# Kernel optimization log

Measured on AMD Instinct MI355X. Metric: run time of the kernel, lower is better.

The kernel has to match this reference:

```python
import jax, jax.numpy as jnp
import numpy as np

HEADS = 4
GROUPS = 32
EPS = 1e-5


def setup_inputs() -> dict:
    key = jax.random.key(0)
    ks = jax.random.split(key, 3)
    B, C, H, W = 8, 256, 32, 32
    x = jax.random.normal(ks[0], (B, C, H, W), dtype=jnp.float32)
    gamma = jnp.ones((C,), jnp.float32)
    beta = jnp.zeros((C,), jnp.float32)
    w_qkv = jax.random.normal(ks[1], (3 * C, C), jnp.float32) * (1.0 / np.sqrt(C))
    b_qkv = jnp.zeros((3 * C,), jnp.float32)
    w_proj = jax.random.normal(ks[2], (C, C), jnp.float32) * (1.0 / np.sqrt(C))
    b_proj = jnp.zeros((C,), jnp.float32)
    return {"x": x, "gamma": gamma, "beta": beta, "w_qkv": w_qkv,
            "b_qkv": b_qkv, "w_proj": w_proj, "b_proj": b_proj}


def group_norm(x, gamma, beta):
    B, C, H, W = x.shape
    xg = x.reshape(B, GROUPS, C // GROUPS, H, W)
    mean = xg.mean(axis=(2, 3, 4), keepdims=True)
    var = xg.var(axis=(2, 3, 4), keepdims=True)
    xg = (xg - mean) * jax.lax.rsqrt(var + EPS)
    xn = xg.reshape(B, C, H, W)
    return xn * gamma[None, :, None, None] + beta[None, :, None, None]


def reference(x, gamma, beta, w_qkv, b_qkv, w_proj, b_proj):
    B, C, H, W = x.shape
    hd = C // HEADS  # head dim
    h = group_norm(x, gamma, beta)
    # 1x1 conv == channel matmul: [B,3C,H,W]
    qkv = jnp.einsum('oc,bchw->bohw', w_qkv, h) + b_qkv[None, :, None, None]
    qkv = qkv.reshape(B, 3, HEADS, hd, H * W)
    q, k, v = qkv[:, 0], qkv[:, 1], qkv[:, 2]  # each [B, heads, hd, HW]
    attn = jnp.einsum('bhci,bhcj->bhij', q, k) * (hd ** -0.5)
    attn = jax.nn.softmax(attn, axis=-1)
    out = jnp.einsum('bhij,bhcj->bhci', attn, v).reshape(B, C, H, W)
    proj = jnp.einsum('oc,bchw->bohw', w_proj, out) + b_proj[None, :, None, None]
    return x + proj
```

## Files before the change

kernel.cpp:

```cpp
#include <hip/hip_runtime.h>
#include <hip/hip_bf16.h>

static constexpr int kC = 256;
static constexpr int kN = 1024;

using s16x8 = __attribute__((ext_vector_type(8))) short;
using f32x4 = __attribute__((ext_vector_type(4))) float;

__device__ inline f32x4 mfma16(s16x8 a, s16x8 b, f32x4 c) {
  return __builtin_amdgcn_mfma_f32_16x16x32_bf16(a, b, c, 0, 0, 0);
}

__device__ inline unsigned short f2bf(float f) {
  unsigned u = __builtin_bit_cast(unsigned, f);
  u = (u + 0x7fffu + ((u >> 16) & 1u)) >> 16;
  return (unsigned short)u;
}

__device__ inline float exp2_fast(float x) {
  float r;
  asm("v_exp_f32 %0, %1" : "=v"(r) : "v"(x));
  return r;
}

__device__ inline unsigned cvt_pk_bf16(float lo, float hi) {
  unsigned r;
  asm("v_cvt_pk_bf16_f32 %0, %1, %2" : "=v"(r) : "v"(lo), "v"(hi));
  return r;
}

static constexpr float kQScale = 0.18033688011112042f;

__global__ __launch_bounds__(256) void prep_kernel(
    const float* __restrict__ x, const float* __restrict__ gamma,
    const float* __restrict__ beta, unsigned short* __restrict__ hTp,
    const float* __restrict__ wq, const float* __restrict__ wp,
    unsigned short* __restrict__ Wqp, unsigned short* __restrict__ Wpp) {
  if (blockIdx.x < 128) {
    const int tid = blockIdx.x * 256 + threadIdx.x;
    const float* src;
    unsigned short* dst;
    if (tid < 24576) {
      const int fragid = tid >> 6, lane = tid & 63;
      const int Mt = fragid >> 3, kt = fragid & 7;
      src = wq + (size_t)(Mt * 16 + (lane & 15)) * 256 + kt * 32 + (lane >> 4) * 8;
      dst = Wqp + (size_t)tid * 8;
    } else {
      const int id = tid - 24576;
      const int fragid = id >> 6, lane = id & 63;
      const int Mt = fragid >> 3, kt = fragid & 7;
      src = wp + (size_t)(Mt * 16 + (lane & 15)) * 256 + kt * 32 + (lane >> 4) * 8;
      dst = Wpp + (size_t)id * 8;
    }
    const float4 f0 = *(const float4*)src;
    const float4 f1 = *(const float4*)(src + 4);
    ushort4 o0, o1;
    o0.x = f2bf(f0.x); o0.y = f2bf(f0.y); o0.z = f2bf(f0.z); o0.w = f2bf(f0.w);
    o1.x = f2bf(f1.x); o1.y = f2bf(f1.y); o1.z = f2bf(f1.z); o1.w = f2bf(f1.w);
    *(ushort4*)dst = o0;
    *(ushort4*)(dst + 4) = o1;
    return;
  }

  const int bg = blockIdx.x - 128;
  const int b = bg >> 5, g = bg & 31;
  const size_t base = ((size_t)b * kC + (size_t)g * 8) * kN;
  const float4* __restrict__ x4 = (const float4*)(x + base);
  const int t = threadIdx.x;

  float vv[8][4];
  float s = 0.f, ss = 0.f;
#pragma unroll
  for (int i = 0; i < 8; ++i) {
    const float4 v = x4[t + 256 * i];
    vv[i][0] = v.x; vv[i][1] = v.y; vv[i][2] = v.z; vv[i][3] = v.w;
    s += v.x + v.y + v.z + v.w;
    ss += v.x * v.x + v.y * v.y + v.z * v.z + v.w * v.w;
  }
#pragma unroll
  for (int off = 32; off > 0; off >>= 1) {
    s += __shfl_xor(s, off);
    ss += __shfl_xor(ss, off);
  }
  __shared__ float rs[4], rss[4];
  const int wave = t >> 6, lane = t & 63;
  if (lane == 0) { rs[wave] = s; rss[wave] = ss; }
  __syncthreads();
  s = rs[0] + rs[1] + rs[2] + rs[3];
  ss = rss[0] + rss[1] + rss[2] + rss[3];
  const float mean = s * (1.f / 8192.f);
  const float var = ss * (1.f / 8192.f) - mean * mean;
  const float rinv = rsqrtf(var + 1e-5f);
  float ga[8], be[8];
#pragma unroll
  for (int i = 0; i < 8; ++i) {
    ga[i] = gamma[g * 8 + i] * rinv;
    be[i] = beta[g * 8 + i] - mean * ga[i];
  }
  const int kt = g >> 2, gq = g & 3;
#pragma unroll
  for (int r = 0; r < 4; ++r) {
    const int pos = 4 * t + r;
    const int nt = pos >> 4, lp = pos & 15;
    unsigned short* dst =
        hTp + ((size_t)((b * 64 + nt) * 8 + kt) * 64 + (gq * 16 + lp)) * 8;
    ushort4 o0, o1;
    o0.x = f2bf(vv[0][r] * ga[0] + be[0]);
    o0.y = f2bf(vv[1][r] * ga[1] + be[1]);
    o0.z = f2bf(vv[2][r] * ga[2] + be[2]);
    o0.w = f2bf(vv[3][r] * ga[3] + be[3]);
    o1.x = f2bf(vv[4][r] * ga[4] + be[4]);
    o1.y = f2bf(vv[5][r] * ga[5] + be[5]);
    o1.z = f2bf(vv[6][r] * ga[6] + be[6]);
    o1.w = f2bf(vv[7][r] * ga[7] + be[7]);
    *(ushort4*)dst = o0;
    *(ushort4*)(dst + 4) = o1;
  }
}

__device__ inline void gload(const s16x8* __restrict__ Af,
                             const s16x8* __restrict__ Bf,
                             int Mt0, int Nt0, int kt, int lane,
                             s16x8 (&a)[4], s16x8 (&bb)[2]) {
#pragma unroll
  for (int mt = 0; mt < 4; ++mt)
    a[mt] = Af[((size_t)(Mt0 + mt) * 8 + kt) * 64 + lane];
#pragma unroll
  for (int nt = 0; nt < 2; ++nt)
    bb[nt] = Bf[((size_t)(Nt0 + nt) * 8 + kt) * 64 + lane];
}

__device__ inline void gmfma(const s16x8 (&a)[4], const s16x8 (&bb)[2],
                             f32x4 (&acc)[4][2], bool swap) {
  if (swap) {
#pragma unroll
    for (int mt = 0; mt < 4; ++mt)
#pragma unroll
      for (int nt = 0; nt < 2; ++nt)
        acc[mt][nt] = mfma16(bb[nt], a[mt], acc[mt][nt]);
  } else {
#pragma unroll
    for (int mt = 0; mt < 4; ++mt)
#pragma unroll
      for (int nt = 0; nt < 2; ++nt)
        acc[mt][nt] = mfma16(a[mt], bb[nt], acc[mt][nt]);
  }
}

template <int MT128, bool PROJ>
__global__ __launch_bounds__(256) void gemm_pk_kernel(
    const unsigned short* __restrict__ Wp, const float* __restrict__ bias,
    const unsigned short* __restrict__ Bp,
    unsigned short* __restrict__ Qp, unsigned short* __restrict__ Kp,
    unsigned short* __restrict__ Vp,
    const float* __restrict__ res, float* __restrict__ outp) {
  constexpr int CPX = MT128 * 16;
  const int bid = blockIdx.x;
  const int swz = (bid & 7) * CPX + (bid >> 3);
  const int b = swz / CPX, rr = swz % CPX;
  const int mb = rr >> 4, nb = rr & 15;
  const int t = threadIdx.x;
  const int wave = t >> 6, lane = t & 63;
  const int li = lane & 15, grp = lane >> 4;
  const int m0 = mb * 128 + (wave >> 1) * 64;
  const int n0 = nb * 64 + (wave & 1) * 32;
  const bool swap = (!PROJ) && (mb >= 4);
  const int Mt0 = m0 >> 4;
  const int Nt0 = b * 64 + (n0 >> 4);
  const s16x8* __restrict__ Af = (const s16x8*)Wp;
  const s16x8* __restrict__ Bf = (const s16x8*)Bp;

  f32x4 acc[4][2];
#pragma unroll
  for (int mt = 0; mt < 4; ++mt)
#pragma unroll
    for (int nt = 0; nt < 2; ++nt) acc[mt][nt] = f32x4{0.f, 0.f, 0.f, 0.f};

  s16x8 sa[3][4], sb[3][2];
  gload(Af, Bf, Mt0, Nt0, 0, lane, sa[0], sb[0]);
  gload(Af, Bf, Mt0, Nt0, 1, lane, sa[1], sb[1]);
#pragma unroll
  for (int kt = 0; kt < 8; ++kt) {
    if (kt + 2 < 8)
      gload(Af, Bf, Mt0, Nt0, kt + 2, lane, sa[(kt + 2) % 3], sb[(kt + 2) % 3]);
    gmfma(sa[kt % 3], sb[kt % 3], acc, swap);
  }

  if (PROJ) {
#pragma unroll
    for (int mt = 0; mt < 4; ++mt) {
      const int mbase = m0 + mt * 16 + 4 * grp;
      const float4 bv = *(const float4*)(bias + mbase);
      const float bvr[4] = {bv.x, bv.y, bv.z, bv.w};
#pragma unroll
      for (int nt = 0; nt < 2; ++nt) {
        const int pos = n0 + nt * 16 + li;
#pragma unroll
        for (int r = 0; r < 4; ++r) {
          const size_t ob = ((size_t)(b * 256 + mbase + r)) * 1024 + pos;
          outp[ob] = acc[mt][nt][r] + bvr[r] + res[ob];
        }
      }
    }
  } else if (!swap) {
    unsigned short* __restrict__ Tp = (mb < 2) ? Qp : Kp;
    const float qs = (mb < 2) ? kQScale : 1.0f;
#pragma unroll
    for (int mt = 0; mt < 4; ++mt) {
      const int mbase = m0 + mt * 16;
      const int head = (mbase >> 6) & 3;
      const int bh = b * 4 + head;
      const int c16 = mbase & 63;
      const int ks = c16 >> 5;
      const int grpp = ((c16 >> 3) + (grp >> 1)) & 3;
      const float4 bv = *(const float4*)(bias + mbase + 4 * grp);
#pragma unroll
      for (int nt = 0; nt < 2; ++nt) {
        const int pt = (n0 >> 4) + nt;
        ushort4 o;
        o.x = f2bf((acc[mt][nt][0] + bv.x) * qs);
        o.y = f2bf((acc[mt][nt][1] + bv.y) * qs);
        o.z = f2bf((acc[mt][nt][2] + bv.z) * qs);
        o.w = f2bf((acc[mt][nt][3] + bv.w) * qs);
        *(ushort4*)(Tp + (size_t)bh * 65536 +
                    ((size_t)(pt * 2 + ks) * 64 + grpp * 16 + li) * 8 +
                    (grp & 1) * 4) = o;
      }
    }
  } else {
#pragma unroll
    for (int mt = 0; mt < 4; ++mt) {
      const int mbase = m0 + mt * 16;
      const int head = (mbase >> 6) & 3;
      const int bh = b * 4 + head;
      const int ct = (mbase & 63) >> 4;
      const float bvc = bias[mbase + li];
      const int kvt = n0 >> 5;
#pragma unroll
      for (int nt = 0; nt < 2; ++nt) {
        const int grpv = (nt * 2 + (grp >> 1)) & 3;
        ushort4 o;
        o.x = f2bf(acc[mt][nt][0] + bvc);
        o.y = f2bf(acc[mt][nt][1] + bvc);
        o.z = f2bf(acc[mt][nt][2] + bvc);
        o.w = f2bf(acc[mt][nt][3] + bvc);
        *(ushort4*)(Vp + (size_t)bh * 65536 +
                    ((size_t)(ct * 32 + kvt) * 64 + grpv * 16 + li) * 8 +
                    (grp & 1) * 4) = o;
      }
    }
  }
}

__global__ __launch_bounds__(256) void attn_mfma_kernel(
    const unsigned short* __restrict__ Qp, const unsigned short* __restrict__ Kp,
    const unsigned short* __restrict__ Vp, unsigned short* __restrict__ aoTp) {
  __shared__ unsigned short P_lds[4][16][56];
  const int bid = blockIdx.x;
  const int swz = (bid & 7) * 64 + (bid >> 3);
  const int bh = swz >> 4, qb = swz & 15;
  const int b = bh >> 2, head = bh & 3;
  const int t = threadIdx.x;
  const int wave = t >> 6, lane = t & 63;
  const int li = lane & 15, grp = lane >> 4;
  const int q0 = qb * 64 + wave * 16;
  const unsigned short* __restrict__ Qb = Qp + (size_t)bh * 65536;
  const unsigned short* __restrict__ Kb = Kp + (size_t)bh * 65536;
  const unsigned short* __restrict__ Vb = Vp + (size_t)bh * 65536;

  s16x8 qf[2];
#pragma unroll
  for (int ks = 0; ks < 2; ++ks)
    qf[ks] = *(const s16x8*)(Qb + (((q0 >> 4) * 2 + ks) * 64 + lane) * 8);

  f32x4 O[4];
#pragma unroll
  for (int ct = 0; ct < 4; ++ct) O[ct] = f32x4{0.f, 0.f, 0.f, 0.f};
  f32x4 lvec = f32x4{0.f, 0.f, 0.f, 0.f};
  float m_run = -1.0e30f;

  auto loadK = [&](int it, s16x8 (&kk)[2][2]) {
#pragma unroll
    for (int mt = 0; mt < 2; ++mt)
#pragma unroll
      for (int ks = 0; ks < 2; ++ks)
        kk[mt][ks] = *(const s16x8*)(
            Kb + ((size_t)((it * 2 + mt) * 2 + ks) * 64 + lane) * 8);
  };
  auto loadV = [&](int it, s16x8 (&vv)[4]) {
#pragma unroll
    for (int ct = 0; ct < 4; ++ct)
      vv[ct] = *(const s16x8*)(Vb + ((size_t)(ct * 32 + it) * 64 + lane) * 8);
  };
  auto qkt = [&](const s16x8 (&kk)[2][2], f32x4 (&s)[2]) {
#pragma unroll
    for (int mt = 0; mt < 2; ++mt) {
      s[mt] = mfma16(kk[mt][0], qf[0], f32x4{0.f, 0.f, 0.f, 0.f});
      s[mt] = mfma16(kk[mt][1], qf[1], s[mt]);
    }
  };
  auto smaxpv = [&](f32x4 (&s)[2], const s16x8 (&vv)[4]) {
    const float A = fmaxf(fmaxf(s[0][0], s[0][1]), s[0][2]);
    const float B = fmaxf(fmaxf(s[0][3], s[1][0]), s[1][1]);
    const float C = fmaxf(fmaxf(s[1][2], s[1][3]), A);
    float pm = fmaxf(B, C);
    pm = fmaxf(pm, __shfl_xor(pm, 16));
    pm = fmaxf(pm, __shfl_xor(pm, 32));
    if (!__all(pm <= m_run + 8.0f)) {
      const float mnew = fmaxf(m_run, pm);
      const float f = exp2_fast(m_run - mnew);
      m_run = mnew;
      lvec *= f;
#pragma unroll
      for (int ct = 0; ct < 4; ++ct) O[ct] *= f;
    }
    f32x4 p[2];
#pragma unroll
    for (int mt = 0; mt < 2; ++mt) {
#pragma unroll
      for (int r = 0; r < 4; ++r) p[mt][r] = exp2_fast(s[mt][r] - m_run);
      lvec += p[mt];
    }
#pragma unroll
    for (int mt = 0; mt < 2; ++mt) {
      uint2 cc;
      cc.x = cvt_pk_bf16(p[mt][0], p[mt][1]);
      cc.y = cvt_pk_bf16(p[mt][2], p[mt][3]);
      *(uint2*)&P_lds[wave][li][16 * mt + 4 * grp] = cc;
    }
    const s16x8 pf = *(const s16x8*)&P_lds[wave][li][8 * grp];
#pragma unroll
    for (int ct = 0; ct < 4; ++ct) O[ct] = mfma16(vv[ct], pf, O[ct]);
  };

  s16x8 k0[2][2], k1[2][2], v0[4], v1[4];
  loadK(0, k0);
  loadV(0, v0);
  f32x4 sc[2];
  qkt(k0, sc);
  loadK(1, k1);

#pragma unroll 1
  for (int h2 = 0; h2 < 16; ++h2) {
    const int tt = 2 * h2;
    loadV(tt + 1, v1);
    f32x4 sn[2];
    qkt(k1, sn);
    loadK(tt + 2, k0);
    smaxpv(sc, v0);
    loadV(tt + 2, v0);
    f32x4 s2[2];
    qkt(k0, s2);
    loadK(tt + 3, k1);
    smaxpv(sn, v1);
    sc[0] = s2[0];
    sc[1] = s2[1];
  }

  float lt = lvec[0] + lvec[1] + lvec[2] + lvec[3];
  lt += __shfl_xor(lt, 16);
  lt += __shfl_xor(lt, 32);
  const float rinv = 1.f / lt;
#pragma unroll
  for (int ct = 0; ct < 4; ++ct) {
    const int ktp = head * 2 + (ct >> 1);
    const int grpp = ((ct & 1) * 2 + (grp >> 1)) & 3;
    ushort4 o;
    o.x = f2bf(O[ct][0] * rinv);
    o.y = f2bf(O[ct][1] * rinv);
    o.z = f2bf(O[ct][2] * rinv);
    o.w = f2bf(O[ct][3] * rinv);
    *(ushort4*)(aoTp +
                ((size_t)((b * 64 + (q0 >> 4)) * 8 + ktp) * 64 + grpp * 16 + li) * 8 +
                (grp & 1) * 4) = o;
  }
}

extern "C" void kernel_launch(void* const* d_in, const int* in_sizes, int n_in,
                              void* d_out, int out_size, void* d_ws, size_t ws_size,
                              hipStream_t stream) {
  const float* x      = (const float*)d_in[0];
  const float* gamma  = (const float*)d_in[1];
  const float* beta   = (const float*)d_in[2];
  const float* w_qkv  = (const float*)d_in[3];
  const float* b_qkv  = (const float*)d_in[4];
  const float* w_proj = (const float*)d_in[5];
  const float* b_proj = (const float*)d_in[6];
  float* out = (float*)d_out;

  unsigned short* ws = (unsigned short*)d_ws;
  unsigned short* Wqp  = ws;
  unsigned short* Wpp  = Wqp + 196608;
  unsigned short* hTp  = Wpp + 65536;
  unsigned short* Qp   = hTp + 2097152;
  unsigned short* Kp   = Qp + 2097152;
  unsigned short* Vp   = Kp + 2097152;
  unsigned short* aoTp = Vp + 2097152;

  hipLaunchKernelGGL(prep_kernel, dim3(384), dim3(256), 0, stream,
                     x, gamma, beta, hTp, w_qkv, w_proj, Wqp, Wpp);
  hipLaunchKernelGGL((gemm_pk_kernel<6, false>), dim3(768), dim3(256), 0, stream,
                     Wqp, b_qkv, hTp, Qp, Kp, Vp, nullptr, nullptr);
  hipLaunchKernelGGL(attn_mfma_kernel, dim3(512), dim3(256), 0, stream,
                     Qp, Kp, Vp, aoTp);
  hipLaunchKernelGGL((gemm_pk_kernel<2, true>), dim3(256), dim3(256), 0, stream,
                     Wpp, b_proj, aoTp, nullptr, nullptr, nullptr, x, out);
}
```

Measured before the change: 43.06 us.

## Fuse output projection into attention kernel via LDS-staged attention output

The attention kernel now uses 512-thread blocks that cover all four heads for 32 query positions. The normalized attention output is staged in shared memory and multiplied by the projection weights in the same kernel, with the bias and residual added there. This removes a kernel launch and the global write and read of the intermediate attention output. In exchange there are half as many blocks, larger blocks, a block-wide barrier, and more LDS per block, which may lower occupancy and parallelism in the attention phase.

```diff
diff --git a/kernel.cpp b/kernel.cpp
--- a/kernel.cpp
+++ b/kernel.cpp
@@ -147,24 +147,21 @@
   }
 }
 
-template <int MT128, bool PROJ>
-__global__ __launch_bounds__(256) void gemm_pk_kernel(
+__global__ __launch_bounds__(256) void gemm_qkv_kernel(
     const unsigned short* __restrict__ Wp, const float* __restrict__ bias,
     const unsigned short* __restrict__ Bp,
     unsigned short* __restrict__ Qp, unsigned short* __restrict__ Kp,
-    unsigned short* __restrict__ Vp,
-    const float* __restrict__ res, float* __restrict__ outp) {
-  constexpr int CPX = MT128 * 16;
+    unsigned short* __restrict__ Vp) {
   const int bid = blockIdx.x;
-  const int swz = (bid & 7) * CPX + (bid >> 3);
-  const int b = swz / CPX, rr = swz % CPX;
+  const int swz = (bid & 7) * 96 + (bid >> 3);
+  const int b = swz / 96, rr = swz % 96;
   const int mb = rr >> 4, nb = rr & 15;
   const int t = threadIdx.x;
   const int wave = t >> 6, lane = t & 63;
   const int li = lane & 15, grp = lane >> 4;
   const int m0 = mb * 128 + (wave >> 1) * 64;
   const int n0 = nb * 64 + (wave & 1) * 32;
-  const bool swap = (!PROJ) && (mb >= 4);
+  const bool swap = mb >= 4;
   const int Mt0 = m0 >> 4;
   const int Nt0 = b * 64 + (n0 >> 4);
   const s16x8* __restrict__ Af = (const s16x8*)Wp;
@@ -186,23 +183,7 @@
     gmfma(sa[kt % 3], sb[kt % 3], acc, swap);
   }
 
-  if (PROJ) {
-#pragma unroll
-    for (int mt = 0; mt < 4; ++mt) {
-      const int mbase = m0 + mt * 16 + 4 * grp;
-      const float4 bv = *(const float4*)(bias + mbase);
-      const float bvr[4] = {bv.x, bv.y, bv.z, bv.w};
-#pragma unroll
-      for (int nt = 0; nt < 2; ++nt) {
-        const int pos = n0 + nt * 16 + li;
-#pragma unroll
-        for (int r = 0; r < 4; ++r) {
-          const size_t ob = ((size_t)(b * 256 + mbase + r)) * 1024 + pos;
-          outp[ob] = acc[mt][nt][r] + bvr[r] + res[ob];
-        }
-      }
-    }
-  } else if (!swap) {
+  if (!swap) {
     unsigned short* __restrict__ Tp = (mb < 2) ? Qp : Kp;
     const float qs = (mb < 2) ? kQScale : 1.0f;
 #pragma unroll
@@ -252,18 +233,22 @@
   }
 }
 
-__global__ __launch_bounds__(256) void attn_mfma_kernel(
+__global__ __launch_bounds__(512) void attn_proj_kernel(
     const unsigned short* __restrict__ Qp, const unsigned short* __restrict__ Kp,
-    const unsigned short* __restrict__ Vp, unsigned short* __restrict__ aoTp) {
-  __shared__ unsigned short P_lds[4][16][56];
+    const unsigned short* __restrict__ Vp, const unsigned short* __restrict__ Wpp,
+    const float* __restrict__ bpj, const float* __restrict__ x,
+    float* __restrict__ out) {
+  __shared__ unsigned short P_lds[8][16][56];
+  __shared__ __align__(16) unsigned short Ex[2][8][64][8];
   const int bid = blockIdx.x;
-  const int swz = (bid & 7) * 64 + (bid >> 3);
-  const int bh = swz >> 4, qb = swz & 15;
-  const int b = bh >> 2, head = bh & 3;
+  const int swz = (bid & 7) * 32 + (bid >> 3);
+  const int b = swz >> 5, qb = swz & 31;
   const int t = threadIdx.x;
-  const int wave = t >> 6, lane = t & 63;
+  const int w8 = t >> 6, lane = t & 63;
+  const int head = w8 & 3, qh = w8 >> 2;
   const int li = lane & 15, grp = lane >> 4;
-  const int q0 = qb * 64 + wave * 16;
+  const int q0 = qb * 32 + qh * 16;
+  const int bh = b * 4 + head;
   const unsigned short* __restrict__ Qb = Qp + (size_t)bh * 65536;
   const unsigned short* __restrict__ Kb = Kp + (size_t)bh * 65536;
   const unsigned short* __restrict__ Vb = Vp + (size_t)bh * 65536;
@@ -326,9 +311,9 @@
       uint2 cc;
       cc.x = cvt_pk_bf16(p[mt][0], p[mt][1]);
       cc.y = cvt_pk_bf16(p[mt][2], p[mt][3]);
-      *(uint2*)&P_lds[wave][li][16 * mt + 4 * grp] = cc;
-    }
-    const s16x8 pf = *(const s16x8*)&P_lds[wave][li][8 * grp];
+      *(uint2*)&P_lds[w8][li][16 * mt + 4 * grp] = cc;
+    }
+    const s16x8 pf = *(const s16x8*)&P_lds[w8][li][8 * grp];
 #pragma unroll
     for (int ct = 0; ct < 4; ++ct) O[ct] = mfma16(vv[ct], pf, O[ct]);
   };
@@ -370,9 +355,56 @@
     o.y = f2bf(O[ct][1] * rinv);
     o.z = f2bf(O[ct][2] * rinv);
     o.w = f2bf(O[ct][3] * rinv);
-    *(ushort4*)(aoTp +
-                ((size_t)((b * 64 + (q0 >> 4)) * 8 + ktp) * 64 + grpp * 16 + li) * 8 +
-                (grp & 1) * 4) = o;
+    *(ushort4*)&Ex[qh][ktp][grpp * 16 + li][(grp & 1) * 4] = o;
+  }
+  __syncthreads();
+
+  {
+    const int Mt0 = w8 * 2;
+    const s16x8* __restrict__ Af = (const s16x8*)Wpp;
+    f32x4 acc[2][2];
+#pragma unroll
+    for (int mt = 0; mt < 2; ++mt)
+#pragma unroll
+      for (int nt = 0; nt < 2; ++nt) acc[mt][nt] = f32x4{0.f, 0.f, 0.f, 0.f};
+
+    s16x8 pa[3][2];
+    auto loadA = [&](int kt, s16x8 (&a)[2]) {
+#pragma unroll
+      for (int mt = 0; mt < 2; ++mt)
+        a[mt] = Af[((size_t)(Mt0 + mt) * 8 + kt) * 64 + lane];
+    };
+    loadA(0, pa[0]);
+    loadA(1, pa[1]);
+#pragma unroll
+    for (int kt = 0; kt < 8; ++kt) {
+      if (kt + 2 < 8) loadA(kt + 2, pa[(kt + 2) % 3]);
+      s16x8 bb[2];
+#pragma unroll
+      for (int nt = 0; nt < 2; ++nt)
+        bb[nt] = *(const s16x8*)&Ex[nt][kt][lane][0];
+#pragma unroll
+      for (int mt = 0; mt < 2; ++mt)
+#pragma unroll
+        for (int nt = 0; nt < 2; ++nt)
+          acc[mt][nt] = mfma16(pa[kt % 3][mt], bb[nt], acc[mt][nt]);
+    }
+
+#pragma unroll
+    for (int mt = 0; mt < 2; ++mt) {
+      const int mbase = w8 * 32 + mt * 16 + 4 * grp;
+      const float4 bv = *(const float4*)(bpj + mbase);
+      const float bvr[4] = {bv.x, bv.y, bv.z, bv.w};
+#pragma unroll
+      for (int nt = 0; nt < 2; ++nt) {
+        const int pos = qb * 32 + nt * 16 + li;
+#pragma unroll
+        for (int r2 = 0; r2 < 4; ++r2) {
+          const size_t ob = ((size_t)(b * 256 + mbase + r2)) * 1024 + pos;
+          out[ob] = acc[mt][nt][r2] + bvr[r2] + x[ob];
+        }
+      }
+    }
   }
 }
 
@@ -395,14 +427,11 @@
   unsigned short* Qp   = hTp + 2097152;
   unsigned short* Kp   = Qp + 2097152;
   unsigned short* Vp   = Kp + 2097152;
-  unsigned short* aoTp = Vp + 2097152;
 
   hipLaunchKernelGGL(prep_kernel, dim3(384), dim3(256), 0, stream,
                      x, gamma, beta, hTp, w_qkv, w_proj, Wqp, Wpp);
-  hipLaunchKernelGGL((gemm_pk_kernel<6, false>), dim3(768), dim3(256), 0, stream,
-                     Wqp, b_qkv, hTp, Qp, Kp, Vp, nullptr, nullptr);
-  hipLaunchKernelGGL(attn_mfma_kernel, dim3(512), dim3(256), 0, stream,
-                     Qp, Kp, Vp, aoTp);
-  hipLaunchKernelGGL((gemm_pk_kernel<2, true>), dim3(256), dim3(256), 0, stream,
-                     Wpp, b_proj, aoTp, nullptr, nullptr, nullptr, x, out);
-}
+  hipLaunchKernelGGL(gemm_qkv_kernel, dim3(768), dim3(256), 0, stream,
+                     Wqp, b_qkv, hTp, Qp, Kp, Vp);
+  hipLaunchKernelGGL(attn_proj_kernel, dim3(256), dim3(512), 0, stream,
+                     Qp, Kp, Vp, Wpp, b_proj, x, out);
+}
```

New measurement: 42.31 us. About the same (-1.8%).
